# Kernel tuning notes

Measured on AMD Instinct MI355X. Metric: run time of the kernel, lower is better.

The kernel has to match this reference:

```python
import jax, jax.numpy as jnp
import numpy as np

N_NODES = 50000
N_EDGES = 800000
IN_C, HID_C, OUT_C = 128, 128, 64


def setup_inputs() -> dict:
    key = jax.random.key(0)
    k1, k2, k3, k4 = jax.random.split(key, 4)
    x = jax.random.normal(k1, (N_NODES, IN_C), dtype=jnp.float32)
    edge_index = jax.random.randint(k2, (2, N_EDGES), 0, N_NODES, dtype=jnp.int64)
    # Glorot-ish init for weights, zero bias (PyG GCNConv default has bias)
    W1 = jax.random.normal(k3, (IN_C, HID_C), dtype=jnp.float32) * (1.0 / np.sqrt(IN_C))
    b1 = jnp.zeros((HID_C,), dtype=jnp.float32)
    W2 = jax.random.normal(k4, (HID_C, OUT_C), dtype=jnp.float32) * (1.0 / np.sqrt(HID_C))
    b2 = jnp.zeros((OUT_C,), dtype=jnp.float32)
    return {"x": x, "edge_index": edge_index, "W1": W1, "b1": b1, "W2": W2, "b2": b2}


def _gcn_norm(edge_index, num_nodes):
    """PyG gcn_norm: add self-loops, symmetric deg^{-1/2} normalization."""
    loop = jnp.arange(num_nodes, dtype=edge_index.dtype)
    src = jnp.concatenate([edge_index[0], loop])  # [E + N]
    dst = jnp.concatenate([edge_index[1], loop])
    ones = jnp.ones(src.shape[0], dtype=jnp.float32)
    deg = jax.ops.segment_sum(ones, dst, num_segments=num_nodes)  # in-degree incl. self-loop
    dinv = jnp.where(deg > 0, jax.lax.rsqrt(deg), 0.0)
    norm = dinv[src] * dinv[dst]  # [E + N]
    return src, dst, norm


def _gcn_conv(x, W, b, src, dst, norm, num_nodes):
    h = x @ W                                   # [N, C_out] transform first (PyG order)
    msg = h[src] * norm[:, None]                # gather + normalize, [E+N, C_out]
    out = jax.ops.segment_sum(msg, dst, num_segments=num_nodes)  # scatter-add
    return out + b


def reference(x, edge_index, W1, b1, W2, b2):
    N = x.shape[0]
    src, dst, norm = _gcn_norm(edge_index, N)  # graph normalization shared by both layers
    h = jax.nn.relu(_gcn_conv(x, W1, b1, src, dst, norm, N))
    out = _gcn_conv(h, W2, b2, src, dst, norm, N)
    return out
```

## Files before the change

kernel.cpp:

```cpp
#include <hip/hip_runtime.h>
#include <hip/hip_bf16.h>

#define IN_C  128
#define HID_C 128
#define OUT_CC 64
#define BK    128
#define CAPLG 12

using short8  = __attribute__((ext_vector_type(8))) short;
using float4v = __attribute__((ext_vector_type(4))) float;

__device__ __forceinline__ unsigned short f2b(float f) {
    unsigned int u = __float_as_uint(f);
    return (unsigned short)((u + 0x7fffu + ((u >> 16) & 1u)) >> 16);
}
__device__ __forceinline__ unsigned int pack2(float a, float b) {
    return (unsigned int)f2b(a) | ((unsigned int)f2b(b) << 16);
}
__device__ __forceinline__ float2 bf2_to_f2(unsigned int v) {
    float2 r;
    r.x = __uint_as_float(v << 16);
    r.y = __uint_as_float(v & 0xffff0000u);
    return r;
}


__global__ __launch_bounds__(256) void k_bpart(const int* __restrict__ ei,
                                               int* __restrict__ bfill,
                                               int* __restrict__ ebuf, int E, int NBK,
                                               int NCHK,
                                               const float* __restrict__ W1,
                                               const float* __restrict__ W2,
                                               unsigned short* __restrict__ w1f,
                                               unsigned short* __restrict__ w2f) {
    const int t = threadIdx.x;
    if ((int)blockIdx.x >= NCHK) {
        int e = ((int)blockIdx.x - NCHK) * 256 + t;
        if (e < 16384) {
            int j = e & 7, lane = (e >> 3) & 63, ks = (e >> 9) & 3, nt = e >> 11;
            int k = ks * 32 + ((lane >> 4) << 3) + j;
            int n = nt * 16 + (lane & 15);
            w1f[e] = f2b(W1[k * 128 + n]);
        } else if (e < 16384 + 8192) {
            int e2 = e - 16384;
            int j = e2 & 7, lane = (e2 >> 3) & 63, ks = (e2 >> 9) & 3, nt = e2 >> 11;
            int k = ks * 32 + ((lane >> 4) << 3) + j;
            int n = nt * 16 + (lane & 15);
            w2f[e2] = f2b(W2[k * 64 + n]);
        }
        return;
    }
    __shared__ int lh[512];
    __shared__ int lbase[512];
    __shared__ int s_st;
    for (int i = t; i < NBK; i += 256) lh[i] = 0;
    if (t < 64) {
        int ev = ei[2 * t], od = ei[2 * t + 1];
        unsigned long long onz = __ballot(od != 0);
        unsigned long long enz = __ballot(ev != 0);
        if (t == 0) s_st = (onz == 0ull && enz != 0ull) ? 2 : 1;
    }
    __syncthreads();
    const int st = s_st;
    const int base = blockIdx.x * 2048;
    int s[8], d[8];
    #pragma unroll
    for (int j = 0; j < 8; ++j) {
        int i = base + j * 256 + t;
        if (i < E) {
            s[j] = ei[(size_t)st * i];
            d[j] = ei[(size_t)st * ((size_t)E + i)];
            atomicAdd(&lh[d[j] >> 7], 1);
        } else d[j] = -1;
    }
    __syncthreads();
    for (int i = t; i < NBK; i += 256) {
        int c = lh[i];
        lbase[i] = c ? atomicAdd(&bfill[i], c) : 0;
        lh[i] = 0;
    }
    __syncthreads();
    #pragma unroll
    for (int j = 0; j < 8; ++j) {
        if (d[j] >= 0) {
            int b = d[j] >> 7;
            int r = lbase[b] + atomicAdd(&lh[b], 1);
            if (r < (1 << CAPLG))
                ebuf[(b << CAPLG) + r] = s[j] | ((d[j] & (BK - 1)) << 20);
        }
    }
}

__global__ __launch_bounds__(256) void k_blmg1(const int* __restrict__ ebuf,
                                               const int* __restrict__ bfill,
                                               int2* __restrict__ begend,
                                               float* __restrict__ dinv,
                                               int* __restrict__ col,
                                               const float* __restrict__ x,
                                               const unsigned short* __restrict__ w1f,
                                               unsigned short* __restrict__ h,
                                               int N, int NBK) {
    __shared__ unsigned short lds[64 * 136];
    __shared__ int cnt64[64];
    const int t = threadIdx.x;

    if ((int)blockIdx.x < NBK) {
        int* cnt = (int*)lds;
        int* sc  = cnt + BK;
        int* off = sc + BK;
        const int n0 = blockIdx.x * BK;
        const int beg = (int)blockIdx.x << CAPLG;
        const int ecnt = min(bfill[blockIdx.x], 1 << CAPLG);
        if (t < BK) cnt[t] = 0;
        __syncthreads();
        for (int i = t; i < ecnt; i += 256)
            atomicAdd(&cnt[ebuf[beg + i] >> 20], 1);
        __syncthreads();
        if (t < BK) sc[t] = cnt[t];
        __syncthreads();
        for (int o = 1; o < BK; o <<= 1) {
            int v = (t < BK && t >= o) ? sc[t - o] : 0;
            __syncthreads();
            if (t < BK) sc[t] += v;
            __syncthreads();
        }
        if (t < BK) {
            int c = cnt[t];
            off[t] = sc[t] - c;
            if (n0 + t < N) {
                begend[n0 + t] = make_int2(beg + off[t], beg + sc[t]);
                dinv[n0 + t] = rsqrtf((float)c + 1.0f);
            }
            cnt[t] = 0;
        }
        __syncthreads();
        for (int i = t; i < ecnt; i += 256) {
            int e = ebuf[beg + i];
            int dl = e >> 20;
            int p = beg + off[dl] + atomicAdd(&cnt[dl], 1);
            col[p] = e & 0xFFFFF;
        }
        return;
    }

    const int tile = (int)blockIdx.x - NBK;
    const int row0 = tile * 64;
    const int bkt  = row0 >> 7;
    const int half = (row0 >> 6) & 1;
    if (t < 64) cnt64[t] = 0;
    __syncthreads();
    {
        const int ebeg = bkt << CAPLG;
        const int ecnt = min(bfill[bkt], 1 << CAPLG);
        for (int i = t; i < ecnt; i += 256) {
            int dl = ebuf[ebeg + i] >> 20;
            if ((dl >> 6) == half) atomicAdd(&cnt64[dl & 63], 1);
        }
    }
    {
        int r = t >> 2, cc = (t & 3) * 32;
        int grow = row0 + r;
        unsigned int* dst = (unsigned int*)&lds[r * 136 + cc];
        if (grow < N) {
            const float4* src = (const float4*)(x + (size_t)grow * 128 + cc);
            #pragma unroll
            for (int i = 0; i < 8; ++i) {
                float4 v = src[i];
                dst[2 * i]     = pack2(v.x, v.y);
                dst[2 * i + 1] = pack2(v.z, v.w);
            }
        } else {
            #pragma unroll
            for (int i = 0; i < 16; ++i) dst[i] = 0;
        }
    }
    __syncthreads();
    const int w = t >> 6, lane = t & 63;
    const int quad = lane >> 4, m = lane & 15;
    short8 a[4];
    #pragma unroll
    for (int ks = 0; ks < 4; ++ks)
        a[ks] = *(const short8*)&lds[(w * 16 + m) * 136 + ks * 32 + quad * 8];
    float4v acc[8];
    #pragma unroll
    for (int nt = 0; nt < 8; ++nt) acc[nt] = (float4v){0.f, 0.f, 0.f, 0.f};
    const short8* wf = (const short8*)w1f;
    #pragma unroll
    for (int nt = 0; nt < 8; ++nt)
        #pragma unroll
        for (int ks = 0; ks < 4; ++ks)
            acc[nt] = __builtin_amdgcn_mfma_f32_16x16x32_bf16(a[ks], wf[(nt * 4 + ks) * 64 + lane],
                                                              acc[nt], 0, 0, 0);
    float drr[4];
    #pragma unroll
    for (int r = 0; r < 4; ++r) {
        int lr = w * 16 + quad * 4 + r;
        drr[r] = rsqrtf((float)cnt64[lr] + 1.0f);
    }
    #pragma unroll
    for (int nt = 0; nt < 8; ++nt)
        #pragma unroll
        for (int r = 0; r < 4; ++r) {
            int grow = row0 + w * 16 + quad * 4 + r;
            if (grow < N) h[(size_t)grow * 128 + nt * 16 + m] = f2b(acc[nt][r] * drr[r]);
        }
}

#define ACC16(u) { float2 q; \
    q = bf2_to_f2(u.x); a0 += q.x; a1 += q.y; \
    q = bf2_to_f2(u.y); a2 += q.x; a3 += q.y; \
    q = bf2_to_f2(u.z); a4 += q.x; a5 += q.y; \
    q = bf2_to_f2(u.w); a6 += q.x; a7 += q.y; }

#define PIPE_GATHER_S2(FEATP, ROWSTRIDE, LANEOFF) \
    int ee = e + sub; \
    int c0, c1, c2, c3; \
    if (ee + 6 < end) { c0 = col[ee]; c1 = col[ee + 2]; c2 = col[ee + 4]; c3 = col[ee + 6]; } \
    for (; ee + 14 < end; ee += 8) { \
        int p0 = col[ee + 8], p1 = col[ee + 10], p2 = col[ee + 12], p3 = col[ee + 14]; \
        uint4 u0 = FEATP[(size_t)c0 * ROWSTRIDE + LANEOFF]; \
        uint4 u1 = FEATP[(size_t)c1 * ROWSTRIDE + LANEOFF]; \
        uint4 u2 = FEATP[(size_t)c2 * ROWSTRIDE + LANEOFF]; \
        uint4 u3 = FEATP[(size_t)c3 * ROWSTRIDE + LANEOFF]; \
        ACC16(u0) ACC16(u1) ACC16(u2) ACC16(u3) \
        c0 = p0; c1 = p1; c2 = p2; c3 = p3; \
    } \
    if (ee + 6 < end) { \
        uint4 u0 = FEATP[(size_t)c0 * ROWSTRIDE + LANEOFF]; \
        uint4 u1 = FEATP[(size_t)c1 * ROWSTRIDE + LANEOFF]; \
        uint4 u2 = FEATP[(size_t)c2 * ROWSTRIDE + LANEOFF]; \
        uint4 u3 = FEATP[(size_t)c3 * ROWSTRIDE + LANEOFF]; \
        ACC16(u0) ACC16(u1) ACC16(u2) ACC16(u3) \
        ee += 8; \
    } \
    for (; ee < end; ee += 2) { \
        uint4 u = FEATP[(size_t)col[ee] * ROWSTRIDE + LANEOFF]; \
        ACC16(u) \
    }

__global__ __launch_bounds__(512) void k_aggmg2(const uint4* __restrict__ feat,
                                                const int2* __restrict__ begend,
                                                const int* __restrict__ col,
                                                const float* __restrict__ dinv,
                                                const float* __restrict__ b1,
                                                const unsigned short* __restrict__ w2f,
                                                unsigned short* __restrict__ h2, int N) {
    __shared__ unsigned short lds[16 * 136];
    __shared__ float dvs[16];
    const int grp = threadIdx.x >> 5;
    const int l32 = threadIdx.x & 31;
    const int sub = l32 >> 4;
    const int l16 = l32 & 15;
    const int node = blockIdx.x * 16 + grp;
    float a0 = 0.f, a1 = 0.f, a2 = 0.f, a3 = 0.f, a4 = 0.f, a5 = 0.f, a6 = 0.f, a7 = 0.f;
    if (node < N) {
        const float dd = dinv[node];
        if (l32 == 0) dvs[grp] = dd;
        const int2 be = begend[node];
        const int e = be.x, end = be.y;
        if (sub == 0) {
            uint4 sv = feat[(size_t)node * 16 + l16];
            ACC16(sv)
        }
        PIPE_GATHER_S2(feat, 16, l16)
        a0 += __shfl_xor(a0, 16); a1 += __shfl_xor(a1, 16);
        a2 += __shfl_xor(a2, 16); a3 += __shfl_xor(a3, 16);
        a4 += __shfl_xor(a4, 16); a5 += __shfl_xor(a5, 16);
        a6 += __shfl_xor(a6, 16); a7 += __shfl_xor(a7, 16);
        float4 ba = ((const float4*)b1)[2 * l16];
        float4 bb = ((const float4*)b1)[2 * l16 + 1];
        a0 = fmaxf(a0 * dd + ba.x, 0.0f);
        a1 = fmaxf(a1 * dd + ba.y, 0.0f);
        a2 = fmaxf(a2 * dd + ba.z, 0.0f);
        a3 = fmaxf(a3 * dd + ba.w, 0.0f);
        a4 = fmaxf(a4 * dd + bb.x, 0.0f);
        a5 = fmaxf(a5 * dd + bb.y, 0.0f);
        a6 = fmaxf(a6 * dd + bb.z, 0.0f);
        a7 = fmaxf(a7 * dd + bb.w, 0.0f);
    } else if (l32 == 0) dvs[grp] = 0.f;
    if (sub == 0) {
        uint4 o;
        o.x = pack2(a0, a1);
        o.y = pack2(a2, a3);
        o.z = pack2(a4, a5);
        o.w = pack2(a6, a7);
        *(uint4*)&lds[grp * 136 + l16 * 8] = o;
    }
    __syncthreads();
    if (threadIdx.x < 256) {
        const int w = threadIdx.x >> 6, lane = threadIdx.x & 63;
        const int quad = lane >> 4, m = lane & 15;
        short8 a[4];
        #pragma unroll
        for (int ks = 0; ks < 4; ++ks)
            a[ks] = *(const short8*)&lds[m * 136 + ks * 32 + quad * 8];
        float4v acc = (float4v){0.f, 0.f, 0.f, 0.f};
        const short8* wf = (const short8*)w2f;
        #pragma unroll
        for (int ks = 0; ks < 4; ++ks)
            acc = __builtin_amdgcn_mfma_f32_16x16x32_bf16(a[ks], wf[(w * 4 + ks) * 64 + lane],
                                                          acc, 0, 0, 0);
        const int node0 = blockIdx.x * 16;
        #pragma unroll
        for (int r = 0; r < 4; ++r) {
            int gn = node0 + quad * 4 + r;
            if (gn < N) h2[(size_t)gn * 64 + w * 16 + m] = f2b(acc[r] * dvs[quad * 4 + r]);
        }
    }
}

__global__ __launch_bounds__(256) void k_agg64(const uint4* __restrict__ feat,
                                               const int2* __restrict__ begend,
                                               const int* __restrict__ col,
                                               const float* __restrict__ dinv,
                                               const float* __restrict__ bias,
                                               float* __restrict__ out, int N) {
    const int grp = threadIdx.x >> 4;
    const int l16 = threadIdx.x & 15;
    const int sub = l16 >> 3;
    const int l8  = l16 & 7;
    const int node = blockIdx.x * 16 + grp;
    if (node >= N) return;
    const float dd = dinv[node];
    const int2 be = begend[node];
    const int e = be.x, end = be.y;
    float a0 = 0.f, a1 = 0.f, a2 = 0.f, a3 = 0.f, a4 = 0.f, a5 = 0.f, a6 = 0.f, a7 = 0.f;
    if (sub == 0) {
        uint4 sv = feat[(size_t)node * 8 + l8];
        ACC16(sv)
    }
    PIPE_GATHER_S2(feat, 8, l8)
    a0 += __shfl_xor(a0, 8); a1 += __shfl_xor(a1, 8);
    a2 += __shfl_xor(a2, 8); a3 += __shfl_xor(a3, 8);
    a4 += __shfl_xor(a4, 8); a5 += __shfl_xor(a5, 8);
    a6 += __shfl_xor(a6, 8); a7 += __shfl_xor(a7, 8);
    if (sub == 0) {
        float4 ba = ((const float4*)bias)[2 * l8];
        float4 bb = ((const float4*)bias)[2 * l8 + 1];
        float4 o1, o2;
        o1.x = a0 * dd + ba.x;
        o1.y = a1 * dd + ba.y;
        o1.z = a2 * dd + ba.z;
        o1.w = a3 * dd + ba.w;
        o2.x = a4 * dd + bb.x;
        o2.y = a5 * dd + bb.y;
        o2.z = a6 * dd + bb.z;
        o2.w = a7 * dd + bb.w;
        float4* op = (float4*)out + (size_t)node * 16 + 2 * l8;
        op[0] = o1;
        op[1] = o2;
    }
}

extern "C" void kernel_launch(void* const* d_in, const int* in_sizes, int n_in,
                              void* d_out, int out_size, void* d_ws, size_t ws_size,
                              hipStream_t stream) {
    const float* x  = (const float*)d_in[0];
    const int*   ei = (const int*)d_in[1];
    const float* W1 = (const float*)d_in[2];
    const float* b1 = (const float*)d_in[3];
    const float* W2 = (const float*)d_in[4];
    const float* b2 = (const float*)d_in[5];

    const int N = in_sizes[0] / IN_C;
    const int E = in_sizes[1] / 2;
    const int NBK  = (N + BK - 1) / BK;
    const int NCHK = (E + 2047) / 2048;
    const int NT1  = (N + 63) / 64;

    char* ws = (char*)d_ws;
    int*            bfill   = (int*)(ws + 64);
    int2*           begend  = (int2*)(ws + 4096);
    float*          dinv    = (float*)(ws + 404480);
    unsigned short* w1f     = (unsigned short*)(ws + 604672);
    unsigned short* w2f     = (unsigned short*)(ws + 637440);
    int*            ebuf    = (int*)(ws + 655360);
    int*            col     = (int*)(ws + 7061504);
    unsigned short* h       = (unsigned short*)(ws + 13467904);
    unsigned short* h2      = (unsigned short*)(ws + 26267904);

    hipMemsetAsync(bfill, 0, NBK * sizeof(int), stream);

    k_bpart<<<NCHK + 96, 256, 0, stream>>>(ei, bfill, ebuf, E, NBK, NCHK,
                                           W1, W2, w1f, w2f);

    k_blmg1<<<NBK + NT1, 256, 0, stream>>>(ebuf, bfill, begend, dinv, col,
                                           x, w1f, h, N, NBK);

    k_aggmg2<<<(N + 15) / 16, 512, 0, stream>>>((const uint4*)h, begend, col, dinv, b1,
                                                w2f, h2, N);

    k_agg64<<<(N + 15) / 16, 256, 0, stream>>>((const uint4*)h2, begend, col, dinv, b2,
                                               (float*)d_out, N);
}
```

Measured before the change: 164.3 us.

## Halve threads per node in both aggregation kernels; split layer-1 gather into two passes

The fused layer-1 aggregate-plus-GEMM kernel now uses 16 threads per node instead of 32 and gathers the 128 hidden features in two sequential halves of 64, with 256 threads per block and all four waves doing the MFMA. The layer-2 aggregation drops the two-way edge split and uses 8 threads per node with a serial 4-way pipelined gather, covering 32 nodes per block. The aim is fewer idle threads, less shuffle-reduce overhead and lower launch width. In exchange each thread runs a longer dependent gather chain, and the layer-1 kernel walks each node's edge list twice.

```diff
diff --git a/kernel.cpp b/kernel.cpp
--- a/kernel.cpp
+++ b/kernel.cpp
@@ -211,6 +211,31 @@
     q = bf2_to_f2(u.y); a2 += q.x; a3 += q.y; \
     q = bf2_to_f2(u.z); a4 += q.x; a5 += q.y; \
     q = bf2_to_f2(u.w); a6 += q.x; a7 += q.y; }
+
+#define PIPE_GATHER(FEATP, ROWSTRIDE, LANEOFF) \
+    int c0, c1, c2, c3; \
+    if (e + 4 <= end) { c0 = col[e]; c1 = col[e + 1]; c2 = col[e + 2]; c3 = col[e + 3]; } \
+    for (; e + 8 <= end; e += 4) { \
+        int p0 = col[e + 4], p1 = col[e + 5], p2 = col[e + 6], p3 = col[e + 7]; \
+        uint4 u0 = FEATP[(size_t)c0 * ROWSTRIDE + LANEOFF]; \
+        uint4 u1 = FEATP[(size_t)c1 * ROWSTRIDE + LANEOFF]; \
+        uint4 u2 = FEATP[(size_t)c2 * ROWSTRIDE + LANEOFF]; \
+        uint4 u3 = FEATP[(size_t)c3 * ROWSTRIDE + LANEOFF]; \
+        ACC16(u0) ACC16(u1) ACC16(u2) ACC16(u3) \
+        c0 = p0; c1 = p1; c2 = p2; c3 = p3; \
+    } \
+    if (e + 4 <= end) { \
+        uint4 u0 = FEATP[(size_t)c0 * ROWSTRIDE + LANEOFF]; \
+        uint4 u1 = FEATP[(size_t)c1 * ROWSTRIDE + LANEOFF]; \
+        uint4 u2 = FEATP[(size_t)c2 * ROWSTRIDE + LANEOFF]; \
+        uint4 u3 = FEATP[(size_t)c3 * ROWSTRIDE + LANEOFF]; \
+        ACC16(u0) ACC16(u1) ACC16(u2) ACC16(u3) \
+        e += 4; \
+    } \
+    for (; e < end; ++e) { \
+        uint4 u = FEATP[(size_t)col[e] * ROWSTRIDE + LANEOFF]; \
+        ACC16(u) \
+    }
 
 #define PIPE_GATHER_S2(FEATP, ROWSTRIDE, LANEOFF) \
     int ee = e + sub; \
@@ -238,7 +263,7 @@
         ACC16(u) \
     }
 
-__global__ __launch_bounds__(512) void k_aggmg2(const uint4* __restrict__ feat,
+__global__ __launch_bounds__(256) void k_aggmg2(const uint4* __restrict__ feat,
                                                 const int2* __restrict__ begend,
                                                 const int* __restrict__ col,
                                                 const float* __restrict__ dinv,
@@ -247,28 +272,34 @@
                                                 unsigned short* __restrict__ h2, int N) {
     __shared__ unsigned short lds[16 * 136];
     __shared__ float dvs[16];
-    const int grp = threadIdx.x >> 5;
-    const int l32 = threadIdx.x & 31;
-    const int sub = l32 >> 4;
-    const int l16 = l32 & 15;
+    const int grp = threadIdx.x >> 4;
+    const int l16 = threadIdx.x & 15;
+    const int sub = l16 >> 3;
+    const int l8  = l16 & 7;
     const int node = blockIdx.x * 16 + grp;
+    float dd = 0.f;
+    int ebeg = 0, eend = 0;
+    if (node < N) {
+        dd = dinv[node];
+        if (l16 == 0) dvs[grp] = dd;
+        int2 be = begend[node];
+        ebeg = be.x; eend = be.y;
+    } else if (l16 == 0) dvs[grp] = 0.f;
+
     float a0 = 0.f, a1 = 0.f, a2 = 0.f, a3 = 0.f, a4 = 0.f, a5 = 0.f, a6 = 0.f, a7 = 0.f;
     if (node < N) {
-        const float dd = dinv[node];
-        if (l32 == 0) dvs[grp] = dd;
-        const int2 be = begend[node];
-        const int e = be.x, end = be.y;
+        const int e = ebeg, end = eend;
         if (sub == 0) {
-            uint4 sv = feat[(size_t)node * 16 + l16];
+            uint4 sv = feat[(size_t)node * 16 + l8];
             ACC16(sv)
         }
-        PIPE_GATHER_S2(feat, 16, l16)
-        a0 += __shfl_xor(a0, 16); a1 += __shfl_xor(a1, 16);
-        a2 += __shfl_xor(a2, 16); a3 += __shfl_xor(a3, 16);
-        a4 += __shfl_xor(a4, 16); a5 += __shfl_xor(a5, 16);
-        a6 += __shfl_xor(a6, 16); a7 += __shfl_xor(a7, 16);
-        float4 ba = ((const float4*)b1)[2 * l16];
-        float4 bb = ((const float4*)b1)[2 * l16 + 1];
+        { PIPE_GATHER_S2(feat, 16, l8) }
+        a0 += __shfl_xor(a0, 8); a1 += __shfl_xor(a1, 8);
+        a2 += __shfl_xor(a2, 8); a3 += __shfl_xor(a3, 8);
+        a4 += __shfl_xor(a4, 8); a5 += __shfl_xor(a5, 8);
+        a6 += __shfl_xor(a6, 8); a7 += __shfl_xor(a7, 8);
+        float4 ba = ((const float4*)b1)[2 * l8];
+        float4 bb = ((const float4*)b1)[2 * l8 + 1];
         a0 = fmaxf(a0 * dd + ba.x, 0.0f);
         a1 = fmaxf(a1 * dd + ba.y, 0.0f);
         a2 = fmaxf(a2 * dd + ba.z, 0.0f);
@@ -277,35 +308,64 @@
         a5 = fmaxf(a5 * dd + bb.y, 0.0f);
         a6 = fmaxf(a6 * dd + bb.z, 0.0f);
         a7 = fmaxf(a7 * dd + bb.w, 0.0f);
-    } else if (l32 == 0) dvs[grp] = 0.f;
+    }
     if (sub == 0) {
         uint4 o;
         o.x = pack2(a0, a1);
         o.y = pack2(a2, a3);
         o.z = pack2(a4, a5);
         o.w = pack2(a6, a7);
-        *(uint4*)&lds[grp * 136 + l16 * 8] = o;
-    }
-    __syncthreads();
-    if (threadIdx.x < 256) {
-        const int w = threadIdx.x >> 6, lane = threadIdx.x & 63;
-        const int quad = lane >> 4, m = lane & 15;
-        short8 a[4];
-        #pragma unroll
-        for (int ks = 0; ks < 4; ++ks)
-            a[ks] = *(const short8*)&lds[m * 136 + ks * 32 + quad * 8];
-        float4v acc = (float4v){0.f, 0.f, 0.f, 0.f};
-        const short8* wf = (const short8*)w2f;
-        #pragma unroll
-        for (int ks = 0; ks < 4; ++ks)
-            acc = __builtin_amdgcn_mfma_f32_16x16x32_bf16(a[ks], wf[(w * 4 + ks) * 64 + lane],
-                                                          acc, 0, 0, 0);
-        const int node0 = blockIdx.x * 16;
-        #pragma unroll
-        for (int r = 0; r < 4; ++r) {
-            int gn = node0 + quad * 4 + r;
-            if (gn < N) h2[(size_t)gn * 64 + w * 16 + m] = f2b(acc[r] * dvs[quad * 4 + r]);
-        }
+        *(uint4*)&lds[grp * 136 + l8 * 8] = o;
+    }
+    a0 = a1 = a2 = a3 = a4 = a5 = a6 = a7 = 0.f;
+    if (node < N) {
+        const int e = ebeg, end = eend;
+        if (sub == 0) {
+            uint4 sv = feat[(size_t)node * 16 + 8 + l8];
+            ACC16(sv)
+        }
+        { PIPE_GATHER_S2(feat, 16, (8 + l8)) }
+        a0 += __shfl_xor(a0, 8); a1 += __shfl_xor(a1, 8);
+        a2 += __shfl_xor(a2, 8); a3 += __shfl_xor(a3, 8);
+        a4 += __shfl_xor(a4, 8); a5 += __shfl_xor(a5, 8);
+        a6 += __shfl_xor(a6, 8); a7 += __shfl_xor(a7, 8);
+        float4 ba = ((const float4*)b1)[16 + 2 * l8];
+        float4 bb = ((const float4*)b1)[17 + 2 * l8];
+        a0 = fmaxf(a0 * dd + ba.x, 0.0f);
+        a1 = fmaxf(a1 * dd + ba.y, 0.0f);
+        a2 = fmaxf(a2 * dd + ba.z, 0.0f);
+        a3 = fmaxf(a3 * dd + ba.w, 0.0f);
+        a4 = fmaxf(a4 * dd + bb.x, 0.0f);
+        a5 = fmaxf(a5 * dd + bb.y, 0.0f);
+        a6 = fmaxf(a6 * dd + bb.z, 0.0f);
+        a7 = fmaxf(a7 * dd + bb.w, 0.0f);
+    }
+    if (sub == 1) {
+        uint4 o;
+        o.x = pack2(a0, a1);
+        o.y = pack2(a2, a3);
+        o.z = pack2(a4, a5);
+        o.w = pack2(a6, a7);
+        *(uint4*)&lds[grp * 136 + (8 + l8) * 8] = o;
+    }
+    __syncthreads();
+    const int w = threadIdx.x >> 6, lane = threadIdx.x & 63;
+    const int quad = lane >> 4, m = lane & 15;
+    short8 a[4];
+    #pragma unroll
+    for (int ks = 0; ks < 4; ++ks)
+        a[ks] = *(const short8*)&lds[m * 136 + ks * 32 + quad * 8];
+    float4v acc = (float4v){0.f, 0.f, 0.f, 0.f};
+    const short8* wf = (const short8*)w2f;
+    #pragma unroll
+    for (int ks = 0; ks < 4; ++ks)
+        acc = __builtin_amdgcn_mfma_f32_16x16x32_bf16(a[ks], wf[(w * 4 + ks) * 64 + lane],
+                                                      acc, 0, 0, 0);
+    const int node0 = blockIdx.x * 16;
+    #pragma unroll
+    for (int r = 0; r < 4; ++r) {
+        int gn = node0 + quad * 4 + r;
+        if (gn < N) h2[(size_t)gn * 64 + w * 16 + m] = f2b(acc[r] * dvs[quad * 4 + r]);
     }
 }
 
@@ -315,41 +375,37 @@
                                                const float* __restrict__ dinv,
                                                const float* __restrict__ bias,
                                                float* __restrict__ out, int N) {
-    const int grp = threadIdx.x >> 4;
-    const int l16 = threadIdx.x & 15;
-    const int sub = l16 >> 3;
-    const int l8  = l16 & 7;
-    const int node = blockIdx.x * 16 + grp;
+    const int grp = threadIdx.x >> 3;
+    const int l8  = threadIdx.x & 7;
+    const int node = blockIdx.x * 32 + grp;
     if (node >= N) return;
     const float dd = dinv[node];
     const int2 be = begend[node];
-    const int e = be.x, end = be.y;
-    float a0 = 0.f, a1 = 0.f, a2 = 0.f, a3 = 0.f, a4 = 0.f, a5 = 0.f, a6 = 0.f, a7 = 0.f;
-    if (sub == 0) {
+    int e = be.x; const int end = be.y;
+    float a0, a1, a2, a3, a4, a5, a6, a7;
+    {
         uint4 sv = feat[(size_t)node * 8 + l8];
-        ACC16(sv)
-    }
-    PIPE_GATHER_S2(feat, 8, l8)
-    a0 += __shfl_xor(a0, 8); a1 += __shfl_xor(a1, 8);
-    a2 += __shfl_xor(a2, 8); a3 += __shfl_xor(a3, 8);
-    a4 += __shfl_xor(a4, 8); a5 += __shfl_xor(a5, 8);
-    a6 += __shfl_xor(a6, 8); a7 += __shfl_xor(a7, 8);
-    if (sub == 0) {
-        float4 ba = ((const float4*)bias)[2 * l8];
-        float4 bb = ((const float4*)bias)[2 * l8 + 1];
-        float4 o1, o2;
-        o1.x = a0 * dd + ba.x;
-        o1.y = a1 * dd + ba.y;
-        o1.z = a2 * dd + ba.z;
-        o1.w = a3 * dd + ba.w;
-        o2.x = a4 * dd + bb.x;
-        o2.y = a5 * dd + bb.y;
-        o2.z = a6 * dd + bb.z;
-        o2.w = a7 * dd + bb.w;
-        float4* op = (float4*)out + (size_t)node * 16 + 2 * l8;
-        op[0] = o1;
-        op[1] = o2;
-    }
+        float2 q;
+        q = bf2_to_f2(sv.x); a0 = q.x; a1 = q.y;
+        q = bf2_to_f2(sv.y); a2 = q.x; a3 = q.y;
+        q = bf2_to_f2(sv.z); a4 = q.x; a5 = q.y;
+        q = bf2_to_f2(sv.w); a6 = q.x; a7 = q.y;
+    }
+    PIPE_GATHER(feat, 8, l8)
+    float4 ba = ((const float4*)bias)[2 * l8];
+    float4 bb = ((const float4*)bias)[2 * l8 + 1];
+    float4 o1, o2;
+    o1.x = a0 * dd + ba.x;
+    o1.y = a1 * dd + ba.y;
+    o1.z = a2 * dd + ba.z;
+    o1.w = a3 * dd + ba.w;
+    o2.x = a4 * dd + bb.x;
+    o2.y = a5 * dd + bb.y;
+    o2.z = a6 * dd + bb.z;
+    o2.w = a7 * dd + bb.w;
+    float4* op = (float4*)out + (size_t)node * 16 + 2 * l8;
+    op[0] = o1;
+    op[1] = o2;
 }
 
 extern "C" void kernel_launch(void* const* d_in, const int* in_sizes, int n_in,
@@ -387,9 +443,9 @@
     k_blmg1<<<NBK + NT1, 256, 0, stream>>>(ebuf, bfill, begend, dinv, col,
                                            x, w1f, h, N, NBK);
 
-    k_aggmg2<<<(N + 15) / 16, 512, 0, stream>>>((const uint4*)h, begend, col, dinv, b1,
+    k_aggmg2<<<(N + 15) / 16, 256, 0, stream>>>((const uint4*)h, begend, col, dinv, b1,
                                                 w2f, h2, N);
 
-    k_agg64<<<(N + 15) / 16, 256, 0, stream>>>((const uint4*)h2, begend, col, dinv, b2,
+    k_agg64<<<(N + 31) / 32, 256, 0, stream>>>((const uint4*)h2, begend, col, dinv, b2,
                                                (float*)d_out, N);
 }
```

New measurement: 162.8 us. About the same (-0.9%).
